# Kernel optimization log

Hardware: AMD Instinct MI355X
Metric: run time of the kernel (lower is better)

The kernel has to match this reference:

```python
import jax, jax.numpy as jnp
import numpy as np

ALPHA_LEAKY = 0.2
EPS = 1e-10


def setup_inputs() -> dict:
    key = jax.random.key(0)
    k1, k2, k3, k4 = jax.random.split(key, 4)
    N, E, IN_DIM, OUT_DIM = 50000, 800000, 128, 64
    node_features = jax.random.normal(k1, (N, IN_DIM), dtype=jnp.float32)
    edge_index = jax.random.randint(k2, (2, E), 0, N, dtype=jnp.int64)
    # xavier_uniform with gain=1.414
    def xavier(k, shape, gain=1.414):
        fan_in, fan_out = shape[1], shape[0]
        bound = gain * np.sqrt(6.0 / (fan_in + fan_out))
        return jax.random.uniform(k, shape, jnp.float32, -bound, bound)
    W = xavier(k3, (OUT_DIM, IN_DIM))          # nn.Linear weight layout [out, in]
    a = xavier(k4, (1, 2 * OUT_DIM))           # attention vector [1, 2*out]
    return {"node_features": node_features, "edge_index": edge_index, "W": W, "a": a}


def reference(node_features, edge_index, W, a):
    # h = W(node_features): [N, out_dim]
    h = node_features @ W.T
    num_nodes, out_dim = h.shape
    src = edge_index[0]
    tgt = edge_index[1]
    # a @ cat([h_src, h_tgt]) decomposes into per-node partial scores (no [E, 2d] concat)
    s_src = h @ a[0, :out_dim]   # [N]
    s_tgt = h @ a[0, out_dim:]   # [N]
    e = jax.nn.leaky_relu(s_src[src] + s_tgt[tgt], negative_slope=ALPHA_LEAKY)  # [E]
    # segment softmax over incoming edges of each target node
    e_max = jax.ops.segment_max(e, tgt, num_segments=num_nodes)
    e_exp = jnp.exp(e - e_max[tgt])
    e_sum = jax.ops.segment_sum(e_exp, tgt, num_segments=num_nodes)
    attention = e_exp / (e_sum[tgt] + EPS)
    # weighted scatter-add aggregation of source features into targets
    h_prime = jax.ops.segment_sum(h[src] * attention[:, None], tgt, num_segments=num_nodes)
    return jax.nn.elu(h_prime)
```

## Files before the change

kernel.cpp:

```cpp
#include <hip/hip_runtime.h>
#include <math.h>

#define ALPHA_LEAKY 0.2f
#define EPS_F 1e-10f
#define NBMAX 1024

typedef __attribute__((ext_vector_type(8))) short short8;
typedef __attribute__((ext_vector_type(4))) float f32x4;

__device__ __forceinline__ unsigned short bf16_rne(float f) {
    unsigned u = __float_as_uint(f);
    u += 0x7FFFu + ((u >> 16) & 1u);
    return (unsigned short)(u >> 16);
}

__global__ void k_prep(const float* __restrict__ W, uint4* __restrict__ Wbf) {
    int f = blockIdx.x * 256 + threadIdx.x;
    int nt = f >> 8;
    if (nt >= 4) return;
    int l = f & 63, kt = (f >> 6) & 3;
    int nn = nt * 16 + (l & 15);
    int k  = kt * 32 + (l >> 4) * 8;
    const float* wr = W + nn * 128 + k;
    unsigned short b[8];
    #pragma unroll
    for (int j = 0; j < 8; ++j) b[j] = bf16_rne(wr[j]);
    uint4 v;
    v.x = (unsigned)b[0] | ((unsigned)b[1] << 16);
    v.y = (unsigned)b[2] | ((unsigned)b[3] << 16);
    v.z = (unsigned)b[4] | ((unsigned)b[5] << 16);
    v.w = (unsigned)b[6] | ((unsigned)b[7] << 16);
    Wbf[f] = v;
}

__global__ __launch_bounds__(256) void k_gemm(
    const float* __restrict__ X, const uint4* __restrict__ Wbf,
    const float* __restrict__ a, unsigned short* __restrict__ hb,
    float* __restrict__ s_src, float* __restrict__ s_tgt, int n, int nstripes) {
    const int lane = threadIdx.x & 63;
    const int ml = lane & 15, g = lane >> 4;
    short8 bfr[4][4];
    #pragma unroll
    for (int nt = 0; nt < 4; ++nt)
        #pragma unroll
        for (int kt = 0; kt < 4; ++kt) {
            uint4 v = Wbf[(nt * 4 + kt) * 64 + lane];
            bfr[nt][kt] = *(short8*)&v;
        }
    float as[4], at[4];
    #pragma unroll
    for (int nt = 0; nt < 4; ++nt) {
        as[nt] = a[nt * 16 + ml];
        at[nt] = a[64 + nt * 16 + ml];
    }
    for (int stripe = blockIdx.x * 4 + (threadIdx.x >> 6); stripe < nstripes;
         stripe += gridDim.x * 4) {
        const int row0 = stripe * 16;
        const int rrow = min(row0 + ml, n - 1);
        const float* xr = X + (size_t)rrow * 128;
        f32x4 acc[4] = {{0.f,0.f,0.f,0.f},{0.f,0.f,0.f,0.f},
                        {0.f,0.f,0.f,0.f},{0.f,0.f,0.f,0.f}};
        #pragma unroll
        for (int kt = 0; kt < 4; ++kt) {
            float4 x0 = *(const float4*)(xr + kt * 32 + g * 8);
            float4 x1 = *(const float4*)(xr + kt * 32 + g * 8 + 4);
            short8 af;
            af[0] = (short)bf16_rne(x0.x); af[1] = (short)bf16_rne(x0.y);
            af[2] = (short)bf16_rne(x0.z); af[3] = (short)bf16_rne(x0.w);
            af[4] = (short)bf16_rne(x1.x); af[5] = (short)bf16_rne(x1.y);
            af[6] = (short)bf16_rne(x1.z); af[7] = (short)bf16_rne(x1.w);
            #pragma unroll
            for (int nt = 0; nt < 4; ++nt)
                acc[nt] = __builtin_amdgcn_mfma_f32_16x16x32_bf16(
                    af, bfr[nt][kt], acc[nt], 0, 0, 0);
        }
        #pragma unroll
        for (int reg = 0; reg < 4; ++reg) {
            int row = row0 + g * 4 + reg;
            float p = acc[0][reg] * as[0] + acc[1][reg] * as[1] +
                      acc[2][reg] * as[2] + acc[3][reg] * as[3];
            float q = acc[0][reg] * at[0] + acc[1][reg] * at[1] +
                      acc[2][reg] * at[2] + acc[3][reg] * at[3];
            #pragma unroll
            for (int off = 1; off < 16; off <<= 1) {
                p += __shfl_xor(p, off, 64);
                q += __shfl_xor(q, off, 64);
            }
            if (ml == 0 && row < n) { s_src[row] = p; s_tgt[row] = q; }
        }
        #pragma unroll
        for (int nt = 0; nt < 4; ++nt)
            #pragma unroll
            for (int reg = 0; reg < 4; ++reg) {
                int row = row0 + g * 4 + reg;
                if (row < n)
                    hb[(size_t)row * 64 + nt * 16 + ml] = bf16_rne(acc[nt][reg]);
            }
    }
}

__global__ __launch_bounds__(256) void k_hist(
    const int* __restrict__ ei, int* __restrict__ histg, int nb, int E, int epb) {
    __shared__ int hist[NBMAX];
    const int t = threadIdx.x;
    for (int k = t; k < nb; k += 256) hist[k] = 0;
    __syncthreads();
    const int e0 = blockIdx.x * epb, e1 = min(e0 + epb, E);
    for (int e = e0 + t; e < e1; e += 256)
        atomicAdd(&hist[ei[E + e] >> 6], 1);
    __syncthreads();
    int* outp = histg + (size_t)blockIdx.x * nb;
    for (int k = t; k < nb; k += 256) outp[k] = hist[k];
}

__global__ __launch_bounds__(256) void k_colscan(
    int* __restrict__ histg, int* __restrict__ btot, int nb) {
    __shared__ int wsum[4];
    const int bucket = blockIdx.x;
    const int t = threadIdx.x, lane = t & 63, w = t >> 6;
    int v = histg[(size_t)t * nb + bucket];
    int pre = v;
    #pragma unroll
    for (int off = 1; off < 64; off <<= 1) {
        int x = __shfl_up(pre, off, 64);
        if (lane >= off) pre += x;
    }
    if (lane == 63) wsum[w] = pre;
    __syncthreads();
    int wb = 0;
    for (int k = 0; k < w; ++k) wb += wsum[k];
    histg[(size_t)t * nb + bucket] = wb + pre - v;
    if (t == 255) btot[bucket] = wb + pre;
}

__global__ __launch_bounds__(256) void k_bscan(
    const int* __restrict__ btot, int* __restrict__ bstart, int nb, int E) {
    __shared__ int wsum[4];
    int t = threadIdx.x;
    int lane = t & 63, w = t >> 6;
    int v[4]; int sum = 0;
    #pragma unroll
    for (int j = 0; j < 4; ++j) {
        int idx = t * 4 + j;
        v[j] = (idx < nb) ? btot[idx] : 0;
        sum += v[j];
    }
    int pre = sum;
    #pragma unroll
    for (int off = 1; off < 64; off <<= 1) {
        int x = __shfl_up(pre, off, 64);
        if (lane >= off) pre += x;
    }
    if (lane == 63) wsum[w] = pre;
    __syncthreads();
    int wbase = 0;
    for (int k = 0; k < w; ++k) wbase += wsum[k];
    int run = wbase + pre - sum;
    #pragma unroll
    for (int j = 0; j < 4; ++j) {
        int idx = t * 4 + j;
        if (idx < nb) bstart[idx] = run;
        run += v[j];
    }
    if (t == 255) bstart[nb] = E;
}

__global__ __launch_bounds__(256) void k_place(
    const int* __restrict__ ei, const int* __restrict__ histg,
    const int* __restrict__ bstart, int2* __restrict__ st,
    int nb, int E, int epb) {
    __shared__ int cur[NBMAX];
    const int t = threadIdx.x;
    const int* my = histg + (size_t)blockIdx.x * nb;
    for (int k = t; k < nb; k += 256) cur[k] = bstart[k] + my[k];
    __syncthreads();
    const int e0 = blockIdx.x * epb, e1 = min(e0 + epb, E);
    for (int e = e0 + t; e < e1; e += 256) {
        int s  = ei[e];
        int tt = ei[E + e];
        int slot = atomicAdd(&cur[tt >> 6], 1);
        st[slot] = make_int2(s, tt);
    }
}

__global__ __launch_bounds__(256) void k_local(
    const int2* __restrict__ st, const int* __restrict__ bstart,
    int* __restrict__ base, int* __restrict__ deg, int* __restrict__ csr_src,
    int n) {
    __shared__ int hist[64];
    __shared__ int nbase[64];
    const int b = blockIdx.x;
    const int n0 = b << 6;
    const int t = threadIdx.x;
    if (t < 64) hist[t] = 0;
    __syncthreads();
    const int s0 = bstart[b], s1 = bstart[b + 1];
    for (int i = s0 + t; i < s1; i += 256)
        atomicAdd(&hist[st[i].y - n0], 1);
    __syncthreads();
    if (t < 64) {
        int v = hist[t];
        int pre = v;
        #pragma unroll
        for (int off = 1; off < 64; off <<= 1) {
            int x = __shfl_up(pre, off, 64);
            if (t >= off) pre += x;
        }
        int bs = s0 + pre - v;
        nbase[t] = bs;
        if (n0 + t < n) { base[n0 + t] = bs; deg[n0 + t] = v; }
    }
    __syncthreads();
    if (t < 64) hist[t] = nbase[t];
    __syncthreads();
    for (int i = s0 + t; i < s1; i += 256) {
        int2 e = st[i];
        int slot = atomicAdd(&hist[e.y - n0], 1);
        csr_src[slot] = e.x;
    }
}

__device__ __forceinline__ void accum8(float acc[8], uint4 hv, float w) {
    unsigned u[4] = {hv.x, hv.y, hv.z, hv.w};
    #pragma unroll
    for (int i = 0; i < 4; ++i) {
        float lo = __uint_as_float(u[i] << 16);
        float hi = __uint_as_float(u[i] & 0xFFFF0000u);
        acc[2 * i]     = fmaf(w, lo, acc[2 * i]);
        acc[2 * i + 1] = fmaf(w, hi, acc[2 * i + 1]);
    }
}

__global__ __launch_bounds__(256) void k_node(
    const int* __restrict__ base, const int* __restrict__ deg,
    const int* __restrict__ csr_src, const float* __restrict__ s_src,
    const float* __restrict__ s_tgt, const unsigned short* __restrict__ hb,
    float* __restrict__ out, int n) {
    const int lane = threadIdx.x & 63;
    const int node = blockIdx.x * 4 + (threadIdx.x >> 6);
    if (node >= n) return;
    const int b = base[node];
    const int d = deg[node];
    const float st = s_tgt[node];
    const int g = lane >> 3, r = lane & 7;
    float acc[8] = {0.f, 0.f, 0.f, 0.f, 0.f, 0.f, 0.f, 0.f};

    if (d <= 64) {
        int src_l = 0; float w_l = 0.f, v = -INFINITY;
        if (lane < d) {
            src_l = csr_src[b + lane];
            float x = s_src[src_l] + st;
            v = (x > 0.f) ? x : ALPHA_LEAKY * x;
        }
        float m = v;
        #pragma unroll
        for (int off = 32; off > 0; off >>= 1) m = fmaxf(m, __shfl_xor(m, off, 64));
        float ex = (lane < d) ? expf(v - m) : 0.f;
        float sum = ex;
        #pragma unroll
        for (int off = 32; off > 0; off >>= 1) sum += __shfl_xor(sum, off, 64);
        w_l = ex * (1.f / (sum + EPS_F));
        for (int k = 0; k < d; k += 8) {
            int ke = k + g;
            int s   = __shfl(src_l, ke, 64);
            float w = __shfl(w_l,  ke, 64);
            uint4 hv = ((const uint4*)(hb + (size_t)s * 64))[r];
            accum8(acc, hv, w);
        }
    } else {
        float m = -INFINITY;
        for (int c = lane; c < d; c += 64) {
            float x = s_src[csr_src[b + c]] + st;
            x = (x > 0.f) ? x : ALPHA_LEAKY * x;
            m = fmaxf(m, x);
        }
        #pragma unroll
        for (int off = 32; off > 0; off >>= 1) m = fmaxf(m, __shfl_xor(m, off, 64));
        float sum = 0.f;
        for (int c = lane; c < d; c += 64) {
            float x = s_src[csr_src[b + c]] + st;
            x = (x > 0.f) ? x : ALPHA_LEAKY * x;
            sum += expf(x - m);
        }
        #pragma unroll
        for (int off = 32; off > 0; off >>= 1) sum += __shfl_xor(sum, off, 64);
        float inv = 1.f / (sum + EPS_F);
        for (int c0 = 0; c0 < d; c0 += 64) {
            int j = c0 + lane;
            int src_l = 0; float w_l = 0.f;
            if (j < d) {
                src_l = csr_src[b + j];
                float x = s_src[src_l] + st;
                x = (x > 0.f) ? x : ALPHA_LEAKY * x;
                w_l = expf(x - m) * inv;
            }
            int lim = min(64, d - c0);
            for (int k = 0; k < lim; k += 8) {
                int ke = k + g;
                int s   = __shfl(src_l, ke, 64);
                float w = __shfl(w_l,  ke, 64);
                uint4 hv = ((const uint4*)(hb + (size_t)s * 64))[r];
                accum8(acc, hv, w);
            }
        }
    }

    #pragma unroll
    for (int off = 8; off <= 32; off <<= 1) {
        #pragma unroll
        for (int j = 0; j < 8; ++j) acc[j] += __shfl_xor(acc[j], off, 64);
    }
    if (g == 0) {
        float4 o0, o1;
        o0.x = acc[0] > 0.f ? acc[0] : expf(acc[0]) - 1.f;
        o0.y = acc[1] > 0.f ? acc[1] : expf(acc[1]) - 1.f;
        o0.z = acc[2] > 0.f ? acc[2] : expf(acc[2]) - 1.f;
        o0.w = acc[3] > 0.f ? acc[3] : expf(acc[3]) - 1.f;
        o1.x = acc[4] > 0.f ? acc[4] : expf(acc[4]) - 1.f;
        o1.y = acc[5] > 0.f ? acc[5] : expf(acc[5]) - 1.f;
        o1.z = acc[6] > 0.f ? acc[6] : expf(acc[6]) - 1.f;
        o1.w = acc[7] > 0.f ? acc[7] : expf(acc[7]) - 1.f;
        float4* o4 = (float4*)out + (size_t)node * 16;
        o4[r * 2]     = o0;
        o4[r * 2 + 1] = o1;
    }
}

extern "C" void kernel_launch(void* const* d_in, const int* in_sizes, int n_in,
                              void* d_out, int out_size, void* d_ws, size_t ws_size,
                              hipStream_t stream) {
    const float* X  = (const float*)d_in[0];
    const int*   ei = (const int*)d_in[1];
    const float* W  = (const float*)d_in[2];
    const float* a  = (const float*)d_in[3];
    float* out = (float*)d_out;

    const int N = in_sizes[0] / 128;
    const int E = in_sizes[1] / 2;
    const int nb = (N + 63) >> 6;
    const int NBLK = 256;
    const int epb = (E + NBLK - 1) / NBLK;

    char* p = (char*)d_ws;
    unsigned short* hb = (unsigned short*)p; p += (size_t)N * 64 * sizeof(unsigned short);
    uint4* Wbf    = (uint4*)p;  p += 1024 * sizeof(uint4);
    float* s_src  = (float*)p;  p += (size_t)N * sizeof(float);
    float* s_tgt  = (float*)p;  p += (size_t)N * sizeof(float);
    int*   deg    = (int*)p;    p += (size_t)N * sizeof(int);
    int*   base   = (int*)p;    p += (size_t)N * sizeof(int);
    int*   histg  = (int*)p;    p += (size_t)NBLK * nb * sizeof(int);
    int*   btot   = (int*)p;    p += (size_t)nb * sizeof(int);
    int*   bstart = (int*)p;    p += (size_t)(nb + 1) * sizeof(int);
    int*   csr_src= (int*)p;    p += (size_t)E * sizeof(int);
    int2*  st     = (int2*)p;

    const int nstripes = (N + 15) / 16;
    k_prep   <<<4, 256, 0, stream>>>(W, Wbf);
    k_gemm   <<<(nstripes + 3) / 4, 256, 0, stream>>>(X, Wbf, a, hb, s_src, s_tgt, N, nstripes);
    k_hist   <<<NBLK, 256, 0, stream>>>(ei, histg, nb, E, epb);
    k_colscan<<<nb, 256, 0, stream>>>(histg, btot, nb);
    k_bscan  <<<1, 256, 0, stream>>>(btot, bstart, nb, E);
    k_place  <<<NBLK, 256, 0, stream>>>(ei, histg, bstart, st, nb, E, epb);
    k_local  <<<nb, 256, 0, stream>>>(st, bstart, base, deg, csr_src, N);
    k_node   <<<(N + 3) / 4, 256, 0, stream>>>(base, deg, csr_src, s_src, s_tgt, hb, out, N);
}
```

Before: 147.0 us.

## Replace bucketed two-level CSR build with global-atomic degree count and fill

Removes the separate W-conversion kernel by converting W to bf16 inside the GEMM, and folds the per-target degree histogram into the GEMM kernel's tail using global atomics. The multi-pass bucket sort (hist, column scan, bucket scan, place, local sort) is replaced by a per-block scan that reserves ranges with an atomic counter, then a single fill pass using global atomics on per-node cursors. The aim is fewer kernel launches and less intermediate traffic. In exchange it takes more contended global atomics, and neighbour order within a node becomes nondeterministic, which can change float summation order.

```diff
diff --git a/kernel.cpp b/kernel.cpp
--- a/kernel.cpp
+++ b/kernel.cpp
@@ -3,7 +3,6 @@
 
 #define ALPHA_LEAKY 0.2f
 #define EPS_F 1e-10f
-#define NBMAX 1024
 
 typedef __attribute__((ext_vector_type(8))) short short8;
 typedef __attribute__((ext_vector_type(4))) float f32x4;
@@ -14,38 +13,29 @@
     return (unsigned short)(u >> 16);
 }
 
-__global__ void k_prep(const float* __restrict__ W, uint4* __restrict__ Wbf) {
-    int f = blockIdx.x * 256 + threadIdx.x;
-    int nt = f >> 8;
-    if (nt >= 4) return;
-    int l = f & 63, kt = (f >> 6) & 3;
-    int nn = nt * 16 + (l & 15);
-    int k  = kt * 32 + (l >> 4) * 8;
-    const float* wr = W + nn * 128 + k;
-    unsigned short b[8];
-    #pragma unroll
-    for (int j = 0; j < 8; ++j) b[j] = bf16_rne(wr[j]);
-    uint4 v;
-    v.x = (unsigned)b[0] | ((unsigned)b[1] << 16);
-    v.y = (unsigned)b[2] | ((unsigned)b[3] << 16);
-    v.z = (unsigned)b[4] | ((unsigned)b[5] << 16);
-    v.w = (unsigned)b[6] | ((unsigned)b[7] << 16);
-    Wbf[f] = v;
-}
-
 __global__ __launch_bounds__(256) void k_gemm(
-    const float* __restrict__ X, const uint4* __restrict__ Wbf,
+    const float* __restrict__ X, const float* __restrict__ W,
     const float* __restrict__ a, unsigned short* __restrict__ hb,
-    float* __restrict__ s_src, float* __restrict__ s_tgt, int n, int nstripes) {
+    float* __restrict__ s_src, float* __restrict__ s_tgt,
+    const int* __restrict__ ei, int* __restrict__ deg,
+    int n, int nstripes, int E, int epb) {
     const int lane = threadIdx.x & 63;
     const int ml = lane & 15, g = lane >> 4;
+
     short8 bfr[4][4];
     #pragma unroll
     for (int nt = 0; nt < 4; ++nt)
         #pragma unroll
         for (int kt = 0; kt < 4; ++kt) {
-            uint4 v = Wbf[(nt * 4 + kt) * 64 + lane];
-            bfr[nt][kt] = *(short8*)&v;
+            const float* wr = W + (nt * 16 + ml) * 128 + kt * 32 + g * 8;
+            float4 w0 = *(const float4*)wr;
+            float4 w1 = *(const float4*)(wr + 4);
+            short8 bf;
+            bf[0] = (short)bf16_rne(w0.x); bf[1] = (short)bf16_rne(w0.y);
+            bf[2] = (short)bf16_rne(w0.z); bf[3] = (short)bf16_rne(w0.w);
+            bf[4] = (short)bf16_rne(w1.x); bf[5] = (short)bf16_rne(w1.y);
+            bf[6] = (short)bf16_rne(w1.z); bf[7] = (short)bf16_rne(w1.w);
+            bfr[nt][kt] = bf;
         }
     float as[4], at[4];
     #pragma unroll
@@ -53,6 +43,7 @@
         as[nt] = a[nt * 16 + ml];
         at[nt] = a[64 + nt * 16 + ml];
     }
+
     for (int stripe = blockIdx.x * 4 + (threadIdx.x >> 6); stripe < nstripes;
          stripe += gridDim.x * 4) {
         const int row0 = stripe * 16;
@@ -97,28 +88,23 @@
                     hb[(size_t)row * 64 + nt * 16 + ml] = bf16_rne(acc[nt][reg]);
             }
     }
-}
-
-__global__ __launch_bounds__(256) void k_hist(
-    const int* __restrict__ ei, int* __restrict__ histg, int nb, int E, int epb) {
-    __shared__ int hist[NBMAX];
-    const int t = threadIdx.x;
-    for (int k = t; k < nb; k += 256) hist[k] = 0;
-    __syncthreads();
-    const int e0 = blockIdx.x * epb, e1 = min(e0 + epb, E);
-    for (int e = e0 + t; e < e1; e += 256)
-        atomicAdd(&hist[ei[E + e] >> 6], 1);
-    __syncthreads();
-    int* outp = histg + (size_t)blockIdx.x * nb;
-    for (int k = t; k < nb; k += 256) outp[k] = hist[k];
-}
-
-__global__ __launch_bounds__(256) void k_colscan(
-    int* __restrict__ histg, int* __restrict__ btot, int nb) {
+
+    {
+        const int e0 = blockIdx.x * epb;
+        const int e1 = min(e0 + epb, E);
+        for (int e = e0 + (int)threadIdx.x; e < e1; e += 256)
+            atomicAdd(&deg[ei[E + e]], 1);
+    }
+}
+
+__global__ __launch_bounds__(256) void k_alloc(
+    const int* __restrict__ deg, int* __restrict__ cur,
+    int* __restrict__ cnt, int n) {
     __shared__ int wsum[4];
-    const int bucket = blockIdx.x;
+    __shared__ int bbase;
     const int t = threadIdx.x, lane = t & 63, w = t >> 6;
-    int v = histg[(size_t)t * nb + bucket];
+    const int node = blockIdx.x * 256 + t;
+    int v = (node < n) ? deg[node] : 0;
     int pre = v;
     #pragma unroll
     for (int off = 1; off < 64; off <<= 1) {
@@ -127,96 +113,25 @@
     }
     if (lane == 63) wsum[w] = pre;
     __syncthreads();
-    int wb = 0;
+    if (t == 0) {
+        int tot = wsum[0] + wsum[1] + wsum[2] + wsum[3];
+        bbase = atomicAdd(cnt, tot);
+    }
+    __syncthreads();
+    int wb = bbase;
     for (int k = 0; k < w; ++k) wb += wsum[k];
-    histg[(size_t)t * nb + bucket] = wb + pre - v;
-    if (t == 255) btot[bucket] = wb + pre;
-}
-
-__global__ __launch_bounds__(256) void k_bscan(
-    const int* __restrict__ btot, int* __restrict__ bstart, int nb, int E) {
-    __shared__ int wsum[4];
-    int t = threadIdx.x;
-    int lane = t & 63, w = t >> 6;
-    int v[4]; int sum = 0;
-    #pragma unroll
-    for (int j = 0; j < 4; ++j) {
-        int idx = t * 4 + j;
-        v[j] = (idx < nb) ? btot[idx] : 0;
-        sum += v[j];
-    }
-    int pre = sum;
-    #pragma unroll
-    for (int off = 1; off < 64; off <<= 1) {
-        int x = __shfl_up(pre, off, 64);
-        if (lane >= off) pre += x;
-    }
-    if (lane == 63) wsum[w] = pre;
-    __syncthreads();
-    int wbase = 0;
-    for (int k = 0; k < w; ++k) wbase += wsum[k];
-    int run = wbase + pre - sum;
-    #pragma unroll
-    for (int j = 0; j < 4; ++j) {
-        int idx = t * 4 + j;
-        if (idx < nb) bstart[idx] = run;
-        run += v[j];
-    }
-    if (t == 255) bstart[nb] = E;
-}
-
-__global__ __launch_bounds__(256) void k_place(
-    const int* __restrict__ ei, const int* __restrict__ histg,
-    const int* __restrict__ bstart, int2* __restrict__ st,
-    int nb, int E, int epb) {
-    __shared__ int cur[NBMAX];
-    const int t = threadIdx.x;
-    const int* my = histg + (size_t)blockIdx.x * nb;
-    for (int k = t; k < nb; k += 256) cur[k] = bstart[k] + my[k];
-    __syncthreads();
-    const int e0 = blockIdx.x * epb, e1 = min(e0 + epb, E);
-    for (int e = e0 + t; e < e1; e += 256) {
+    if (node < n) cur[node] = wb + pre - v;
+}
+
+__global__ __launch_bounds__(256) void k_fill(
+    const int* __restrict__ ei, int* __restrict__ cur,
+    int* __restrict__ csr_src, int E) {
+    const int stride = gridDim.x * 256;
+    for (int e = blockIdx.x * 256 + (int)threadIdx.x; e < E; e += stride) {
         int s  = ei[e];
         int tt = ei[E + e];
-        int slot = atomicAdd(&cur[tt >> 6], 1);
-        st[slot] = make_int2(s, tt);
-    }
-}
-
-__global__ __launch_bounds__(256) void k_local(
-    const int2* __restrict__ st, const int* __restrict__ bstart,
-    int* __restrict__ base, int* __restrict__ deg, int* __restrict__ csr_src,
-    int n) {
-    __shared__ int hist[64];
-    __shared__ int nbase[64];
-    const int b = blockIdx.x;
-    const int n0 = b << 6;
-    const int t = threadIdx.x;
-    if (t < 64) hist[t] = 0;
-    __syncthreads();
-    const int s0 = bstart[b], s1 = bstart[b + 1];
-    for (int i = s0 + t; i < s1; i += 256)
-        atomicAdd(&hist[st[i].y - n0], 1);
-    __syncthreads();
-    if (t < 64) {
-        int v = hist[t];
-        int pre = v;
-        #pragma unroll
-        for (int off = 1; off < 64; off <<= 1) {
-            int x = __shfl_up(pre, off, 64);
-            if (t >= off) pre += x;
-        }
-        int bs = s0 + pre - v;
-        nbase[t] = bs;
-        if (n0 + t < n) { base[n0 + t] = bs; deg[n0 + t] = v; }
-    }
-    __syncthreads();
-    if (t < 64) hist[t] = nbase[t];
-    __syncthreads();
-    for (int i = s0 + t; i < s1; i += 256) {
-        int2 e = st[i];
-        int slot = atomicAdd(&hist[e.y - n0], 1);
-        csr_src[slot] = e.x;
+        int slot = atomicAdd(&cur[tt], 1);
+        csr_src[slot] = s;
     }
 }
 
@@ -232,15 +147,15 @@
 }
 
 __global__ __launch_bounds__(256) void k_node(
-    const int* __restrict__ base, const int* __restrict__ deg,
+    const int* __restrict__ deg, const int* __restrict__ cur,
     const int* __restrict__ csr_src, const float* __restrict__ s_src,
     const float* __restrict__ s_tgt, const unsigned short* __restrict__ hb,
     float* __restrict__ out, int n) {
     const int lane = threadIdx.x & 63;
     const int node = blockIdx.x * 4 + (threadIdx.x >> 6);
     if (node >= n) return;
-    const int b = base[node];
     const int d = deg[node];
+    const int b = cur[node] - d;
     const float st = s_tgt[node];
     const int g = lane >> 3, r = lane & 7;
     float acc[8] = {0.f, 0.f, 0.f, 0.f, 0.f, 0.f, 0.f, 0.f};
@@ -337,30 +252,25 @@
 
     const int N = in_sizes[0] / 128;
     const int E = in_sizes[1] / 2;
-    const int nb = (N + 63) >> 6;
-    const int NBLK = 256;
-    const int epb = (E + NBLK - 1) / NBLK;
 
     char* p = (char*)d_ws;
     unsigned short* hb = (unsigned short*)p; p += (size_t)N * 64 * sizeof(unsigned short);
-    uint4* Wbf    = (uint4*)p;  p += 1024 * sizeof(uint4);
     float* s_src  = (float*)p;  p += (size_t)N * sizeof(float);
     float* s_tgt  = (float*)p;  p += (size_t)N * sizeof(float);
     int*   deg    = (int*)p;    p += (size_t)N * sizeof(int);
-    int*   base   = (int*)p;    p += (size_t)N * sizeof(int);
-    int*   histg  = (int*)p;    p += (size_t)NBLK * nb * sizeof(int);
-    int*   btot   = (int*)p;    p += (size_t)nb * sizeof(int);
-    int*   bstart = (int*)p;    p += (size_t)(nb + 1) * sizeof(int);
-    int*   csr_src= (int*)p;    p += (size_t)E * sizeof(int);
-    int2*  st     = (int2*)p;
+    int*   cnt    = (int*)p;    p += 4 * sizeof(int);
+    int*   cur    = (int*)p;    p += (size_t)N * sizeof(int);
+    int*   csr_src= (int*)p;
 
     const int nstripes = (N + 15) / 16;
-    k_prep   <<<4, 256, 0, stream>>>(W, Wbf);
-    k_gemm   <<<(nstripes + 3) / 4, 256, 0, stream>>>(X, Wbf, a, hb, s_src, s_tgt, N, nstripes);
-    k_hist   <<<NBLK, 256, 0, stream>>>(ei, histg, nb, E, epb);
-    k_colscan<<<nb, 256, 0, stream>>>(histg, btot, nb);
-    k_bscan  <<<1, 256, 0, stream>>>(btot, bstart, nb, E);
-    k_place  <<<NBLK, 256, 0, stream>>>(ei, histg, bstart, st, nb, E, epb);
-    k_local  <<<nb, 256, 0, stream>>>(st, bstart, base, deg, csr_src, N);
-    k_node   <<<(N + 3) / 4, 256, 0, stream>>>(base, deg, csr_src, s_src, s_tgt, hb, out, N);
-}
+    const int gblk = (nstripes + 3) / 4;
+    const int epb  = (E + gblk - 1) / gblk;
+
+    hipMemsetAsync(deg, 0, (size_t)(N + 4) * sizeof(int), stream);
+    k_gemm <<<gblk, 256, 0, stream>>>(X, W, a, hb, s_src, s_tgt, ei, deg,
+                                      N, nstripes, E, epb);
+    k_alloc<<<(N + 255) / 256, 256, 0, stream>>>(deg, cur, cnt, N);
+    k_fill <<<1024, 256, 0, stream>>>(ei, cur, csr_src, E);
+    k_node <<<(N + 3) / 4, 256, 0, stream>>>(deg, cur, csr_src, s_src, s_tgt,
+                                             hb, out, N);
+}
```

New measurement: 207.9 us. 1.41x slower.
